# Kernel optimization log

Hardware: AMD Instinct MI355X
Metric: run time of the kernel (lower is better)

The kernel has to match this reference:

```python
import jax, jax.numpy as jnp
import numpy as np

TOP_K = 2


def setup_inputs() -> dict:
    key = jax.random.key(0)
    k1, k2, k3, k4 = jax.random.split(key, 4)
    B, L, D, F, E = 4, 2048, 1024, 4096, 8
    x = jax.random.normal(k1, (B, L, D), dtype=jnp.float32)
    router_w = jax.random.normal(k2, (D, E), dtype=jnp.float32) * (1.0 / np.sqrt(D))
    w1 = jax.random.normal(k3, (E, D, F), dtype=jnp.float32) * (1.0 / np.sqrt(D))
    w2 = jax.random.normal(k4, (E, F, D), dtype=jnp.float32) * (1.0 / np.sqrt(F))
    return {"x": x, "router_w": router_w, "w1": w1, "w2": w2}


def reference(x, router_w, w1, w2):
    # x: [B, L, D]; router_w: [D, E]; w1: [E, D, F]; w2: [E, F, D]
    B, L, D = x.shape
    E = router_w.shape[1]
    xt = x.reshape(-1, D)                       # [T, D], T = B*L
    router_logits = xt @ router_w               # [T, E] router GEMM
    probs = jax.nn.softmax(router_logits, axis=-1)
    top_w, top_i = jax.lax.top_k(probs, TOP_K)  # [T, k]
    top_w = top_w / jnp.sum(top_w, axis=-1, keepdims=True)  # renormalize top-k
    # dense combine gates: [T, E], zero outside the selected experts
    gates = jnp.sum(jax.nn.one_hot(top_i, E, dtype=xt.dtype) * top_w[..., None], axis=1)
    out = jnp.zeros_like(xt)
    for e in range(E):  # fixed small expert loop (structurally distinct params)
        h = jax.nn.gelu(xt @ w1[e])             # [T, F]
        out = out + gates[:, e:e + 1] * (h @ w2[e])
    return out.reshape(B, L, D)
```

## Files before the change

### kernel.cpp

```cpp
#include <hip/hip_runtime.h>
#include <hip/hip_bf16.h>


#define T_TOK 8192
#define DDIM  1024
#define FDIM  4096
#define NEXP  8
#define RTOT  (T_TOK * 2)
#define RPAD  (RTOT + 128)

#define BM 128
#define BN 128
#define BK 64

typedef __bf16 bf16x8 __attribute__((ext_vector_type(8)));
typedef float  f32x4  __attribute__((ext_vector_type(4)));

__device__ __forceinline__ float gelu_fast(float x) {
  float x2 = x * x;
  float v = x * __builtin_fmaf(0.10294480f, x2, 2.30211416f);
  float e = __builtin_amdgcn_exp2f(-v);
  return x * __builtin_amdgcn_rcpf(1.f + e);
}

__device__ __forceinline__ float b2f(unsigned short u) {
  return __uint_as_float(((unsigned)u) << 16);
}

#define GLOBAL_TO_LDS16(gp, lp)                                                   \
  __builtin_amdgcn_global_load_lds((const __attribute__((address_space(1))) void*)(gp), \
                                   (__attribute__((address_space(3))) void*)(lp), 16, 0, 0)

__global__ __launch_bounds__(256) void transpose_cast_both(const float* __restrict__ w1,
                                                           const float* __restrict__ w2,
                                                           __hip_bfloat16* __restrict__ w1t,
                                                           __hip_bfloat16* __restrict__ w2t) {
  __shared__ __hip_bfloat16 tileT[64 * 72];
  int bid = blockIdx.x;
  const float* in; __hip_bfloat16* outp; int Rr, Cc;
  if (bid < NEXP * 1024) { in = w1; outp = w1t; Rr = DDIM; Cc = FDIM; }
  else { bid -= NEXP * 1024; in = w2; outp = w2t; Rr = FDIM; Cc = DDIM; }
  int tilesC = Cc >> 6;
  int per = (Rr >> 6) * tilesC;
  int e = bid / per, rem = bid % per;
  int tr = rem / tilesC, tc = rem % tilesC;
  const float* ip = in + (size_t)e * Rr * Cc + (size_t)(tr * 64) * Cc + tc * 64;
  __hip_bfloat16* op = outp + (size_t)e * Rr * Cc + (size_t)(tc * 64) * Rr + tr * 64;
  int tid = threadIdx.x;
  int cbase = (tid & 15) * 4;
  int rbase = (tid >> 4) * 2;
#pragma unroll
  for (int p = 0; p < 2; p++) {
    int r0 = rbase + p * 32;
    float4 va = *(const float4*)(ip + (size_t)r0 * Cc + cbase);
    float4 vb = *(const float4*)(ip + (size_t)(r0 + 1) * Cc + cbase);
    const float* fa = &va.x;
    const float* fb = &vb.x;
#pragma unroll
    for (int i = 0; i < 4; i++) {
      union { __hip_bfloat16 h[2]; unsigned u; } pk;
      pk.h[0] = __float2bfloat16(fa[i]);
      pk.h[1] = __float2bfloat16(fb[i]);
      *(unsigned*)(&tileT[(cbase + i) * 72 + r0]) = pk.u;
    }
  }
  __syncthreads();
  int rr = tid >> 2, sb = (tid & 3) * 16;
  const __hip_bfloat16* src = tileT + rr * 72 + sb;
  __hip_bfloat16* dst = op + (size_t)rr * Rr + sb;
  uint4 v0 = *(const uint4*)(src);
  uint4 v1 = *(const uint4*)(src + 8);
  *(uint4*)(dst) = v0;
  *(uint4*)(dst + 8) = v1;
}

__global__ __launch_bounds__(256) void router_kernel(const float* __restrict__ x,
                                                     const float* __restrict__ rw,
                                                     int* __restrict__ counts,
                                                     int* __restrict__ pair_e,
                                                     int* __restrict__ pair_slot,
                                                     float* __restrict__ pair_gate) {
  int lane = threadIdx.x & 63;
  int wid = threadIdx.x >> 6;
  int t = blockIdx.x * 4 + wid;
  const float* xr = x + (size_t)t * DDIM;
  float acc[NEXP];
#pragma unroll
  for (int e = 0; e < NEXP; e++) acc[e] = 0.f;
  for (int d0 = lane * 4; d0 < DDIM; d0 += 256) {
    float4 xv = *(const float4*)(xr + d0);
    const float* r0 = rw + (size_t)d0 * NEXP;
#pragma unroll
    for (int e = 0; e < NEXP; e++)
      acc[e] += xv.x * r0[e] + xv.y * r0[NEXP + e] + xv.z * r0[2 * NEXP + e] + xv.w * r0[3 * NEXP + e];
  }
#pragma unroll
  for (int e = 0; e < NEXP; e++) {
#pragma unroll
    for (int m = 32; m > 0; m >>= 1) acc[e] += __shfl_xor(acc[e], m, 64);
  }
  if (lane == 0) {
    int e1 = 0; float l1 = acc[0];
    for (int e = 1; e < NEXP; e++) if (acc[e] > l1) { l1 = acc[e]; e1 = e; }
    int e2 = -1; float l2 = -1e30f;
    for (int e = 0; e < NEXP; e++) { if (e == e1) continue; if (acc[e] > l2) { l2 = acc[e]; e2 = e; } }
    float g1 = 1.f / (1.f + __expf(l2 - l1));
    float g2 = 1.f - g1;
    int s1 = atomicAdd(&counts[e1], 1);
    int s2 = atomicAdd(&counts[e2], 1);
    pair_e[2 * t] = e1;     pair_slot[2 * t] = s1;     pair_gate[2 * t] = g1;
    pair_e[2 * t + 1] = e2; pair_slot[2 * t + 1] = s2; pair_gate[2 * t + 1] = g2;
  }
}

__global__ __launch_bounds__(256) void gather_kernel(const float* __restrict__ x,
                                                     const int* __restrict__ counts,
                                                     const int* __restrict__ pair_e,
                                                     const int* __restrict__ pair_slot,
                                                     const float* __restrict__ pair_gate,
                                                     __hip_bfloat16* __restrict__ Xg,
                                                     int* __restrict__ trow,
                                                     float* __restrict__ row_gate) {
  int p = blockIdx.x;
  int t = p >> 1;
  int e = pair_e[p];
  int base = 0;
#pragma unroll
  for (int i = 0; i < NEXP; i++) base += (i < e) ? counts[i] : 0;
  int row = base + pair_slot[p];
  const float* xr = x + (size_t)t * DDIM;
  __hip_bfloat16* dst = Xg + (size_t)row * DDIM;
  int i = threadIdx.x * 4;
  float4 v = *(const float4*)(xr + i);
  union { ushort4 u; __hip_bfloat16 h[4]; } o;
  o.h[0] = __float2bfloat16(v.x);
  o.h[1] = __float2bfloat16(v.y);
  o.h[2] = __float2bfloat16(v.z);
  o.h[3] = __float2bfloat16(v.w);
  *(ushort4*)(dst + i) = o.u;
  if (threadIdx.x == 0) { trow[p] = row; row_gate[row] = pair_gate[p]; }
}

template <int EPI>
__global__ __launch_bounds__(256) void moe_gemm(const __hip_bfloat16* __restrict__ A,
                                                const __hip_bfloat16* __restrict__ Bw,
                                                __hip_bfloat16* __restrict__ Pout,
                                                const int* __restrict__ counts,
                                                const float* __restrict__ row_gate,
                                                int K, int N) {
  const int MT = T_TOK / BM;
  const int NT = N / BN;
  int bid = blockIdx.x;
  int e = bid / (MT * NT);
  int rem = bid % (MT * NT);
  const int GM = 16;
  int width = GM * NT;
  int group = rem / width;
  int gm0 = group * GM;
  int gsize = (MT - gm0 < GM) ? (MT - gm0) : GM;
  int mt = gm0 + (rem % gsize);
  int nt = (rem % width) / gsize;

  int n_e = counts[e];
  if (mt * BM >= n_e) return;
  int row0 = 0;
  for (int i = 0; i < NEXP; i++) row0 += (i < e) ? counts[i] : 0;
  int m_start = row0 + mt * BM;
  int row_end = row0 + n_e;

  const __hip_bfloat16* Abase = A + (size_t)m_start * K;
  const __hip_bfloat16* Bbase = Bw + (size_t)e * N * K + (size_t)(nt * BN) * K;

  __shared__ alignas(16) __hip_bfloat16 As[BM * BK];
  __shared__ alignas(16) __hip_bfloat16 Bs[BN * BK];

  int tid = threadIdx.x;
  int lane = tid & 63, wid = tid >> 6;
  int wm = (wid >> 1) * 64, wn = (wid & 1) * 64;
  int lr = lane & 15;
  int kq8 = (lane >> 4);

  int offA[4][2], offB[4][2];
#pragma unroll
  for (int i = 0; i < 4; i++) {
    int Ra = wm + i * 16 + lr;
    int Rb = wn + i * 16 + lr;
#pragma unroll
    for (int h = 0; h < 2; h++) {
      int kc = kq8 + h * 4;
      offA[i][h] = Ra * BK + ((kc ^ (Ra & 7)) * 8);
      offB[i][h] = Rb * BK + ((kc ^ (Rb & 7)) * 8);
    }
  }
  const __hip_bfloat16* ga[4];
  const __hip_bfloat16* gb[4];
#pragma unroll
  for (int i = 0; i < 4; i++) {
    int q = i * 256 + tid;
    int r = q >> 3, c = (q & 7) ^ (r & 7);
    ga[i] = Abase + (size_t)r * K + c * 8;
    gb[i] = Bbase + (size_t)r * K + c * 8;
  }

  f32x4 acc[4][4];
#pragma unroll
  for (int i = 0; i < 4; i++)
#pragma unroll
    for (int j = 0; j < 4; j++)
#pragma unroll
      for (int r = 0; r < 4; r++) acc[i][j][r] = 0.f;

  for (int kt = 0; kt < K; kt += BK) {
#pragma unroll
    for (int i = 0; i < 4; i++) GLOBAL_TO_LDS16(ga[i], As + (size_t)(i * 256 + wid * 64) * 8);
#pragma unroll
    for (int i = 0; i < 4; i++) GLOBAL_TO_LDS16(gb[i], Bs + (size_t)(i * 256 + wid * 64) * 8);
#pragma unroll
    for (int i = 0; i < 4; i++) { ga[i] += BK; gb[i] += BK; }
    __syncthreads();
#pragma unroll
    for (int h = 0; h < 2; h++) {
      bf16x8 af[4], bfr[4];
#pragma unroll
      for (int i = 0; i < 4; i++) af[i] = *(const bf16x8*)(As + offA[i][h]);
#pragma unroll
      for (int j = 0; j < 4; j++) bfr[j] = *(const bf16x8*)(Bs + offB[j][h]);
#pragma unroll
      for (int i = 0; i < 4; i++)
#pragma unroll
        for (int j = 0; j < 4; j++)
          acc[i][j] = __builtin_amdgcn_mfma_f32_16x16x32_bf16(af[i], bfr[j], acc[i][j], 0, 0, 0);
    }
    __syncthreads();
  }

  int quad = (lane >> 4) * 4;
#pragma unroll
  for (int i = 0; i < 4; i++) {
#pragma unroll
    for (int r = 0; r < 4; r++) {
      int grow = m_start + wm + i * 16 + quad + r;
      if (grow < row_end) {
        __hip_bfloat16* pp = Pout + (size_t)grow * N + nt * BN + wn + lr;
        if (EPI == 0) {
#pragma unroll
          for (int j = 0; j < 4; j++)
            pp[j * 16] = __float2bfloat16(gelu_fast(acc[i][j][r]));
        } else {
          float g = row_gate[grow];
#pragma unroll
          for (int j = 0; j < 4; j++)
            pp[j * 16] = __float2bfloat16(g * acc[i][j][r]);
        }
      }
    }
  }
}

__global__ __launch_bounds__(256) void combine_kernel(const __hip_bfloat16* __restrict__ P,
                                                      const int* __restrict__ trow,
                                                      float* __restrict__ out) {
  int t = blockIdx.x;
  int r1 = trow[2 * t], r2 = trow[2 * t + 1];
  int d = threadIdx.x * 4;
  ushort4 a = *(const ushort4*)(P + (size_t)r1 * DDIM + d);
  ushort4 b = *(const ushort4*)(P + (size_t)r2 * DDIM + d);
  float4 o;
  o.x = b2f(a.x) + b2f(b.x);
  o.y = b2f(a.y) + b2f(b.y);
  o.z = b2f(a.z) + b2f(b.z);
  o.w = b2f(a.w) + b2f(b.w);
  *(float4*)(out + (size_t)t * DDIM + d) = o;
}

extern "C" void kernel_launch(void* const* d_in, const int* in_sizes, int n_in,
                              void* d_out, int out_size, void* d_ws, size_t ws_size,
                              hipStream_t stream) {
  (void)in_sizes; (void)n_in; (void)out_size; (void)ws_size;
  const float* x  = (const float*)d_in[0];
  const float* rw = (const float*)d_in[1];
  const float* w1 = (const float*)d_in[2];
  const float* w2 = (const float*)d_in[3];
  float* out = (float*)d_out;

  char* ws = (char*)d_ws;
  size_t off = 0;
  auto alloc = [&](size_t bytes) -> char* {
    off = (off + 255) & ~(size_t)255;
    char* p = ws + off;
    off += bytes;
    return p;
  };
  int*   counts    = (int*)alloc(NEXP * 4);
  int*   pair_e    = (int*)alloc((size_t)RTOT * 4);
  int*   pair_slot = (int*)alloc((size_t)RTOT * 4);
  float* pair_gate = (float*)alloc((size_t)RTOT * 4);
  int*   trow      = (int*)alloc((size_t)RTOT * 4);
  float* row_gate  = (float*)alloc((size_t)RTOT * 4);
  __hip_bfloat16* Xg  = (__hip_bfloat16*)alloc((size_t)RPAD * DDIM * 2);
  __hip_bfloat16* w1t = (__hip_bfloat16*)alloc((size_t)NEXP * DDIM * FDIM * 2);
  __hip_bfloat16* w2t = (__hip_bfloat16*)alloc((size_t)NEXP * DDIM * FDIM * 2);
  __hip_bfloat16* H   = (__hip_bfloat16*)alloc((size_t)RPAD * FDIM * 2);
  __hip_bfloat16* P = w1t;

  hipMemsetAsync(counts, 0, NEXP * 4, stream);

  transpose_cast_both<<<2 * NEXP * 1024, 256, 0, stream>>>(w1, w2, w1t, w2t);
  router_kernel<<<T_TOK / 4, 256, 0, stream>>>(x, rw, counts, pair_e, pair_slot, pair_gate);
  gather_kernel<<<RTOT, 256, 0, stream>>>(x, counts, pair_e, pair_slot, pair_gate, Xg, trow, row_gate);

  moe_gemm<0><<<NEXP * (T_TOK / BM) * (FDIM / BN), 256, 0, stream>>>(
      Xg, w1t, H, counts, nullptr, DDIM, FDIM);
  moe_gemm<1><<<NEXP * (T_TOK / BM) * (DDIM / BN), 256, 0, stream>>>(
      H, w2t, P, counts, row_gate, FDIM, DDIM);
  combine_kernel<<<T_TOK, 256, 0, stream>>>(P, trow, out);
}
```

Before: 961.1 us.

## Load A fragments directly from global and double-buffer B in LDS

The MoE grouped GEMM no longer stages the A tile through shared memory. Each wave loads its A fragments straight from global into registers, and the B tile goes through an LDS ping-pong buffer. This removes one of the two barriers per K step and the A LDS traffic. The tile-group swizzle width is also halved. The cost is redundant uncoalesced A reads across the two waves sharing rows, and the double buffer relies on the single remaining barrier to avoid write-after-read hazards.

```diff
diff --git a/kernel.cpp b/kernel.cpp
--- a/kernel.cpp
+++ b/kernel.cpp
@@ -153,7 +153,7 @@
   int bid = blockIdx.x;
   int e = bid / (MT * NT);
   int rem = bid % (MT * NT);
-  const int GM = 16;
+  const int GM = 8;
   int width = GM * NT;
   int group = rem / width;
   int gm0 = group * GM;
@@ -171,8 +171,7 @@
   const __hip_bfloat16* Abase = A + (size_t)m_start * K;
   const __hip_bfloat16* Bbase = Bw + (size_t)e * N * K + (size_t)(nt * BN) * K;
 
-  __shared__ alignas(16) __hip_bfloat16 As[BM * BK];
-  __shared__ alignas(16) __hip_bfloat16 Bs[BN * BK];
+  __shared__ alignas(16) __hip_bfloat16 Bs[2 * BN * BK];
 
   int tid = threadIdx.x;
   int lane = tid & 63, wid = tid >> 6;
@@ -180,27 +179,27 @@
   int lr = lane & 15;
   int kq8 = (lane >> 4);
 
-  int offA[4][2], offB[4][2];
-#pragma unroll
-  for (int i = 0; i < 4; i++) {
-    int Ra = wm + i * 16 + lr;
-    int Rb = wn + i * 16 + lr;
+  int offB[4][2];
+#pragma unroll
+  for (int j = 0; j < 4; j++) {
+    int Rb = wn + j * 16 + lr;
 #pragma unroll
     for (int h = 0; h < 2; h++) {
       int kc = kq8 + h * 4;
-      offA[i][h] = Ra * BK + ((kc ^ (Ra & 7)) * 8);
-      offB[i][h] = Rb * BK + ((kc ^ (Rb & 7)) * 8);
-    }
-  }
-  const __hip_bfloat16* ga[4];
+      offB[j][h] = Rb * BK + ((kc ^ (Rb & 7)) * 8);
+    }
+  }
   const __hip_bfloat16* gb[4];
 #pragma unroll
   for (int i = 0; i < 4; i++) {
     int q = i * 256 + tid;
     int r = q >> 3, c = (q & 7) ^ (r & 7);
-    ga[i] = Abase + (size_t)r * K + c * 8;
     gb[i] = Bbase + (size_t)r * K + c * 8;
   }
+  const __hip_bfloat16* pA[4];
+#pragma unroll
+  for (int i = 0; i < 4; i++)
+    pA[i] = Abase + (size_t)(wm + i * 16 + lr) * K + kq8 * 8;
 
   f32x4 acc[4][4];
 #pragma unroll
@@ -210,28 +209,36 @@
 #pragma unroll
       for (int r = 0; r < 4; r++) acc[i][j][r] = 0.f;
 
-  for (int kt = 0; kt < K; kt += BK) {
-#pragma unroll
-    for (int i = 0; i < 4; i++) GLOBAL_TO_LDS16(ga[i], As + (size_t)(i * 256 + wid * 64) * 8);
-#pragma unroll
-    for (int i = 0; i < 4; i++) GLOBAL_TO_LDS16(gb[i], Bs + (size_t)(i * 256 + wid * 64) * 8);
-#pragma unroll
-    for (int i = 0; i < 4; i++) { ga[i] += BK; gb[i] += BK; }
+  auto phase = [&](__hip_bfloat16* BsB) {
+#pragma unroll
+    for (int i = 0; i < 4; i++) {
+      GLOBAL_TO_LDS16(gb[i], BsB + (size_t)(i * 256 + wid * 64) * 8);
+      gb[i] += BK;
+    }
+    bf16x8 af[4][2];
+#pragma unroll
+    for (int i = 0; i < 4; i++) {
+      af[i][0] = *(const bf16x8*)(pA[i]);
+      af[i][1] = *(const bf16x8*)(pA[i] + 32);
+      pA[i] += BK;
+    }
     __syncthreads();
 #pragma unroll
     for (int h = 0; h < 2; h++) {
-      bf16x8 af[4], bfr[4];
-#pragma unroll
-      for (int i = 0; i < 4; i++) af[i] = *(const bf16x8*)(As + offA[i][h]);
-#pragma unroll
-      for (int j = 0; j < 4; j++) bfr[j] = *(const bf16x8*)(Bs + offB[j][h]);
+      bf16x8 bfr[4];
+#pragma unroll
+      for (int j = 0; j < 4; j++) bfr[j] = *(const bf16x8*)(BsB + offB[j][h]);
 #pragma unroll
       for (int i = 0; i < 4; i++)
 #pragma unroll
         for (int j = 0; j < 4; j++)
-          acc[i][j] = __builtin_amdgcn_mfma_f32_16x16x32_bf16(af[i], bfr[j], acc[i][j], 0, 0, 0);
-    }
-    __syncthreads();
+          acc[i][j] = __builtin_amdgcn_mfma_f32_16x16x32_bf16(af[i][h], bfr[j], acc[i][j], 0, 0, 0);
+    }
+  };
+
+  for (int kt = 0; kt < K; kt += 2 * BK) {
+    phase(Bs);
+    phase(Bs + BN * BK);
   }
 
   int quad = (lane >> 4) * 4;
```

Result: slower. 1.314 ms (+36.7%).
